# Kernel tuning notes

Hardware: AMD Instinct MI355X
Metric: run time of the kernel (lower is better)

Reference implementation:

```python
import jax, jax.numpy as jnp
import numpy as np

B, D, T, H, CHUNK, MAX_REL = 4, 512, 8192, 8, 64, 2
HD = D // H


def setup_inputs() -> dict:
    key = jax.random.key(0)
    ks = jax.random.split(key, 16)
    s = 0.02
    inp = {
        "q": jax.random.normal(ks[0], (B, D, T), jnp.float32),
        "k": jax.random.normal(ks[1], (B, D, T), jnp.float32),
        "v": jax.random.normal(ks[2], (B, D, T), jnp.float32),
        "masks": jnp.ones((B, 1, T), jnp.float32),
        "Wq": jax.random.normal(ks[3], (D, D), jnp.float32) * s,
        "bq": jnp.zeros((D,), jnp.float32),
        "Wk": jax.random.normal(ks[4], (D, D), jnp.float32) * s,
        "bk": jnp.zeros((D,), jnp.float32),
        "Wv": jax.random.normal(ks[5], (D, D), jnp.float32) * s,
        "bv": jnp.zeros((D,), jnp.float32),
        "Wo": jax.random.normal(ks[6], (D, D), jnp.float32) * s,
        "bo": jnp.zeros((D,), jnp.float32),
        "rel_k": jax.random.normal(ks[7], (2 * MAX_REL + 1, HD), jnp.float32) * s,
        "rel_v": jax.random.normal(ks[8], (2 * MAX_REL + 1, HD), jnp.float32) * s,
    }
    return inp


def reference(q, k, v, masks, Wq, bq, Wk, bk, Wv, bv, Wo, bo, rel_k, rel_v):
    n = CHUNK
    g = T // n  # T is a multiple of chunck_size -> no padding branch
    bg = B * g

    # (B, D, T) -> (B, T, D) -> (B*g, n, D) chunking
    qt = jnp.swapaxes(q, 1, 2).reshape(bg, n, D)
    kt = jnp.swapaxes(k, 1, 2).reshape(bg, n, D)
    vt = jnp.swapaxes(v, 1, 2).reshape(bg, n, D)
    cm = jnp.swapaxes(masks, 1, 2).reshape(bg, n)  # per-chunk mask values

    # gen_key_padding_mask: chunks that are entirely zero are un-masked (set to 1)
    all_zero = jnp.sum(cm, axis=-1) == 0.0
    cm_fixed = jnp.where(all_zero[:, None], 1.0, cm)
    kpm = cm_fixed == 0.0  # (bg, n) True = masked key

    # projections (torch Linear: x @ W.T + b)
    qp = qt @ Wq.T + bq
    kp = kt @ Wk.T + bk
    vp = vt @ Wv.T + bv

    qh = qp.reshape(bg, n, H, HD).transpose(0, 2, 1, 3)  # (bg, H, n, hd)
    kh = kp.reshape(bg, n, H, HD).transpose(0, 2, 1, 3)
    vh = vp.reshape(bg, n, H, HD).transpose(0, 2, 1, 3)

    # content-content scores
    attn1 = jnp.einsum('bhqd,bhkd->bhqk', qh, kh)

    # relative position indices: clip(k - q, -max, max) + max
    ridx = jnp.clip(jnp.arange(n)[None, :] - jnp.arange(n)[:, None], -MAX_REL, MAX_REL) + MAX_REL
    rk = rel_k[ridx]  # (n, n, hd)
    rv = rel_v[ridx]  # (n, n, hd)

    # content-position scores
    attn2 = jnp.einsum('bhqd,qkd->bhqk', qh, rk)

    scale = jnp.sqrt(jnp.asarray(HD, jnp.float32))
    attn = (attn1 + attn2) / scale
    attn = jnp.where(kpm[:, None, None, :], -jnp.inf, attn)
    p = jax.nn.softmax(attn, axis=-1)  # (bg, H, n, n)

    w1 = jnp.einsum('bhqk,bhkd->bhqd', p, vh)
    w2 = jnp.einsum('bhqk,qkd->bhqd', p, rv)
    xo = (w1 + w2).transpose(0, 2, 1, 3).reshape(bg, n, D)
    xo = xo @ Wo.T + bo

    out = xo.reshape(B, T, D)
    out = jnp.swapaxes(out, 1, 2)  # (B, D, T)
    return out * masks
```

## Files before the change

kernel.cpp:

```cpp
#include <hip/hip_runtime.h>


typedef __attribute__((ext_vector_type(8))) short short8;
typedef __attribute__((ext_vector_type(4))) float f32x4;
typedef __attribute__((ext_vector_type(2))) unsigned int uint2v;
typedef __attribute__((ext_vector_type(4))) unsigned short ushort4v;

#define DEV static __device__ __forceinline__

DEV unsigned short f2bf(float f) {
  union { float f; unsigned int u; } x; x.f = f;
  unsigned int r = x.u + 0x7fffu + ((x.u >> 16) & 1u);
  return (unsigned short)(r >> 16);
}
DEV float bf2f(unsigned short h) {
  union { unsigned int u; float f; } x; x.u = ((unsigned int)h) << 16;
  return x.f;
}

DEV void gload16(char* lds, const void* g) {
  __builtin_amdgcn_global_load_lds(
      (const __attribute__((address_space(1))) unsigned int*)g,
      (__attribute__((address_space(3))) unsigned int*)lds, 16, 0, 0);
}

constexpr int Bn = 4, Dm = 512, Tn = 8192, NC = 64;
constexpr int Gn = Tn / NC;
constexpr int BG = Bn * Gn;
constexpr int WSZ = Dm * Dm;
constexpr size_t XTSZ = (size_t)Bn * Tn * Dm;

__global__ __launch_bounds__(256) void wcvt3_tiled(
    const float* __restrict__ wq, const float* __restrict__ wk,
    const float* __restrict__ wv, unsigned short* __restrict__ dst) {
  int i = blockIdx.x * 256 + threadIdx.x;
  int m = i >> 16, fi = i & 65535;
  int o = fi >> 7, d = (fi & 127) << 2;
  const float* src = (m == 0) ? wq : (m == 1) ? wk : wv;
  f32x4 v = *(const f32x4*)(src + o * Dm + d);
  ushort4v u;
  u[0] = f2bf(v[0]); u[1] = f2bf(v[1]); u[2] = f2bf(v[2]); u[3] = f2bf(v[3]);
  int doff = m * WSZ + ((o >> 6) << 15) + ((d >> 5) << 11) + ((o & 63) << 5) + (d & 31);
  *(ushort4v*)(dst + doff) = u;
}

__global__ __launch_bounds__(256) void wcvt_row1(
    const float* __restrict__ wo, unsigned short* __restrict__ dst) {
  int i = (blockIdx.x * 256 + threadIdx.x) * 4;
  f32x4 v = *(const f32x4*)(wo + i);
  ushort4v u;
  u[0] = f2bf(v[0]); u[1] = f2bf(v[1]); u[2] = f2bf(v[2]); u[3] = f2bf(v[3]);
  *(ushort4v*)(dst + i) = u;
}

__global__ __launch_bounds__(256) void wcvt_tiled(
    const float* __restrict__ wq, const float* __restrict__ wk,
    const float* __restrict__ wv, const float* __restrict__ wo,
    unsigned short* __restrict__ dst) {
  int i = blockIdx.x * 256 + threadIdx.x;
  int m = i >> 16, fi = i & 65535;
  int o = fi >> 7, d = (fi & 127) << 2;
  const float* src = (m == 0) ? wq : (m == 1) ? wk : (m == 2) ? wv : wo;
  f32x4 v = *(const f32x4*)(src + o * Dm + d);
  ushort4v u;
  u[0] = f2bf(v[0]); u[1] = f2bf(v[1]); u[2] = f2bf(v[2]); u[3] = f2bf(v[3]);
  int doff = m * WSZ + ((o >> 6) << 15) + ((d >> 5) << 11) + ((o & 63) << 5) + (d & 31);
  *(ushort4v*)(dst + doff) = u;
}

__global__ __launch_bounds__(256) void xpose_kernel(
    const float* __restrict__ q, const float* __restrict__ k,
    const float* __restrict__ v, unsigned short* __restrict__ xt) {
  __shared__ unsigned short tile[64 * 65];
  const int tid = threadIdx.x, bid = blockIdx.x;
  const int tz = bid >> 12, rem = bid & 4095;
  const int cid = rem >> 3, dh = rem & 7;
  const int b = cid >> 7, t0 = (cid & 127) * 64, d0 = dh * 64;
  const float* xin = (tz == 0) ? q : (tz == 1) ? k : v;
  const int lane = tid & 63, drow = tid >> 6;
  const size_t base = (size_t)b * Dm * Tn + t0 + lane;
#pragma unroll
  for (int p = 0; p < 16; ++p) {
    int dr = drow + p * 4;
    float f = xin[base + (size_t)(d0 + dr) * Tn];
    tile[lane * 65 + dr] = f2bf(f);
  }
  __syncthreads();
  unsigned short* xb = xt + (size_t)tz * XTSZ + ((size_t)cid << 15) + (dh << 12);
  const int t = tid >> 2, dlo = (tid & 3) * 8;
#pragma unroll
  for (int h = 0; h < 2; ++h) {
    short8 s;
#pragma unroll
    for (int j = 0; j < 8; ++j) s[j] = (short)tile[t * 65 + h * 32 + dlo + j];
    *(short8*)(xb + h * 2048 + t * 32 + dlo) = s;
  }
}

__global__ __launch_bounds__(512, 4)
void qkvproj4_kernel(const float* __restrict__ qx, const float* __restrict__ kx,
                     const float* __restrict__ vx,
                     const unsigned short* __restrict__ wt3,
                     const float* __restrict__ bq, const float* __restrict__ bk,
                     const float* __restrict__ bv,
                     unsigned short* __restrict__ qkvf)
{
  __shared__ char st[65536];
  const int tid = threadIdx.x;
  const int lane = tid & 63, w = tid >> 6;
  const int l15 = lane & 15, lg = lane >> 4;
  const int bid = blockIdx.x;
  const int mat = bid >> 9;
  const int c = bid & 511;
  const int b = c >> 7, t0 = (c & 127) * 64;
  const float* xin = (mat == 0) ? qx : (mat == 1) ? kx : vx;

  const size_t xbase = (size_t)b * Dm * Tn + t0 + lane;
#pragma unroll
  for (int half = 0; half < 2; ++half) {
    float xr[32];
#pragma unroll
    for (int s = 0; s < 4; ++s)
#pragma unroll
      for (int j = 0; j < 8; ++j)
        xr[s * 8 + j] = xin[xbase + (size_t)((half * 4 + s) * 64 + w * 8 + j) * Tn];
#pragma unroll
    for (int s = 0; s < 4; ++s) {
      int d0 = (half * 4 + s) * 64 + w * 8;
      short8 pk;
#pragma unroll
      for (int j = 0; j < 8; ++j) pk[j] = (short)f2bf(xr[s * 8 + j]);
      int off = (lane * 1024 + d0 * 2) ^ ((lane & 15) << 4);
      *(short8*)(st + off) = pk;
    }
  }
  __syncthreads();

  const int h = w;
  const unsigned short* wb = wt3 + (size_t)mat * WSZ + ((size_t)h << 15);
  const int aoff = l15 * 32 + lg * 8;

  f32x4 acc[4][4];
  const f32x4 fzero = {0.f, 0.f, 0.f, 0.f};
#pragma unroll
  for (int mi = 0; mi < 4; ++mi)
#pragma unroll
    for (int ni = 0; ni < 4; ++ni) acc[mi][ni] = fzero;

  short8 bcur[4], bnxt[4];
#pragma unroll
  for (int ni = 0; ni < 4; ++ni)
    bcur[ni] = *(const short8*)(wb + 0 * 2048 + ni * 512 + aoff);

#pragma unroll
  for (int kk = 0; kk < 16; ++kk) {
    if (kk < 15) {
#pragma unroll
      for (int ni = 0; ni < 4; ++ni)
        bnxt[ni] = *(const short8*)(wb + (kk + 1) * 2048 + ni * 512 + aoff);
    }
    short8 af[4];
#pragma unroll
    for (int mi = 0; mi < 4; ++mi) {
      int t = mi * 16 + l15;
      int off = (t * 1024 + (kk * 32 + lg * 8) * 2) ^ ((t & 15) << 4);
      af[mi] = *(const short8*)(st + off);
    }
#pragma unroll
    for (int ni = 0; ni < 4; ++ni)
#pragma unroll
      for (int mi = 0; mi < 4; ++mi)
        acc[mi][ni] = __builtin_amdgcn_mfma_f32_16x16x32_bf16(af[mi], bcur[ni],
                                                              acc[mi][ni], 0, 0, 0);
#pragma unroll
    for (int ni = 0; ni < 4; ++ni) bcur[ni] = bnxt[ni];
  }
  __syncthreads();

  char* ep = st + w * 8192;
  const float* bias = (mat == 0) ? bq : (mat == 1) ? bk : bv;

  if (mat < 2) {
#pragma unroll
    for (int ni = 0; ni < 4; ++ni) {
      float bi = bias[h * 64 + ni * 16 + l15];
      int hd = ni * 16 + l15;
#pragma unroll
      for (int mi = 0; mi < 4; ++mi)
#pragma unroll
        for (int rr = 0; rr < 4; ++rr) {
          int t = mi * 16 + lg * 4 + rr;
          int off = (t * 128 + hd * 2) ^ ((t & 7) << 4);
          *(unsigned short*)(ep + off) = f2bf(acc[mi][ni][rr] + bi);
        }
    }
  } else {
#pragma unroll
    for (int ni = 0; ni < 4; ++ni) {
      float bi = bias[h * 64 + ni * 16 + l15];
      int hd = ni * 16 + l15;
#pragma unroll
      for (int mi = 0; mi < 4; ++mi) {
        unsigned int lo = (unsigned int)f2bf(acc[mi][ni][0] + bi) |
                          ((unsigned int)f2bf(acc[mi][ni][1] + bi) << 16);
        unsigned int hi = (unsigned int)f2bf(acc[mi][ni][2] + bi) |
                          ((unsigned int)f2bf(acc[mi][ni][3] + bi) << 16);
        uint2v pk; pk[0] = lo; pk[1] = hi;
        int tt = mi * 16 + lg * 4;
        int off = (hd * 128 + tt * 2) ^ ((hd & 7) << 4);
        *(uint2v*)(ep + off) = pk;
      }
    }
  }

  unsigned short* dst = qkvf + (size_t)mat * XTSZ + ((size_t)(c * 8 + h) << 12);
#pragma unroll
  for (int it = 0; it < 8; ++it) {
    int p = it * 64 + lane;
    int row = p >> 3, c16 = p & 7;
    short8 val = *(const short8*)(ep + ((row * 128 + c16 * 16) ^ ((row & 7) << 4)));
    *(short8*)(dst + row * 64 + c16 * 8) = val;
  }
}

__global__ __launch_bounds__(64, 3)
void attn3_kernel(const unsigned short* __restrict__ qkvf,
                  const float* __restrict__ masks,
                  const float* __restrict__ relk, const float* __restrict__ relv,
                  unsigned short* __restrict__ xo)
{
  __shared__ char ldsbuf[16384];
  char* regA = ldsbuf;
  char* regB = ldsbuf + 8192;
  const int lane = threadIdx.x;
  const int l15 = lane & 15, lg = lane >> 4;
  const int bid = blockIdx.x;
  const int c = bid >> 3, h = bid & 7;
  const int b = c >> 7, t0 = (c & 127) * 64;
  const size_t base = (size_t)(c * 8 + h) << 12;
  const unsigned short* qp = qkvf + base;
  const unsigned short* kp = qkvf + XTSZ + base;
  const unsigned short* vp = qkvf + 2 * XTSZ + base;

  float cmv = masks[(size_t)b * Tn + t0 + lane];
  unsigned long long nzb = __ballot(cmv != 0.0f);
  unsigned long long kpm = (nzb == 0ull) ? 0ull : __ballot(cmv == 0.0f);

  const f32x4 fzero = {0.f, 0.f, 0.f, 0.f};

#pragma unroll
  for (int it = 0; it < 8; ++it) {
    int p = it * 64 + lane;
    int row = p >> 3, c16 = p & 7;
    int off = (row * 128 + c16 * 16) ^ ((row & 7) << 4);
    *(short8*)(regA + off) = *(const short8*)(qp + row * 64 + c16 * 8);
    *(short8*)(regB + off) = *(const short8*)(kp + row * 64 + c16 * 8);
  }

  f32x4 sacc[4][4];
#pragma unroll
  for (int mi = 0; mi < 4; ++mi)
#pragma unroll
    for (int ni = 0; ni < 4; ++ni) sacc[mi][ni] = fzero;
#pragma unroll
  for (int kk = 0; kk < 2; ++kk) {
    short8 aq[4], bkf[4];
#pragma unroll
    for (int mi = 0; mi < 4; ++mi) {
      int t = mi * 16 + l15;
      int off = (t * 128 + (kk * 32 + lg * 8) * 2) ^ ((t & 7) << 4);
      aq[mi]  = *(const short8*)(regA + off);
      bkf[mi] = *(const short8*)(regB + off);
    }
#pragma unroll
    for (int ni = 0; ni < 4; ++ni)
#pragma unroll
      for (int mi = 0; mi < 4; ++mi)
        sacc[mi][ni] = __builtin_amdgcn_mfma_f32_16x16x32_bf16(aq[mi], bkf[ni], sacc[mi][ni], 0, 0, 0);
  }

  float qr0 = 0, qr1 = 0, qr2 = 0, qr3 = 0, qr4 = 0;
#pragma unroll
  for (int g = 0; g < 8; ++g) {
    short8 q8 = *(const short8*)(regA + ((lane * 128 + g * 16) ^ ((lane & 7) << 4)));
#pragma unroll
    for (int j = 0; j < 8; ++j) {
      float qf = bf2f((unsigned short)q8[j]);
      qr0 += qf * relk[0 * 64 + g * 8 + j];
      qr1 += qf * relk[1 * 64 + g * 8 + j];
      qr2 += qf * relk[2 * 64 + g * 8 + j];
      qr3 += qf * relk[3 * 64 + g * 8 + j];
      qr4 += qf * relk[4 * 64 + g * 8 + j];
    }
  }

#pragma unroll
  for (int it = 0; it < 8; ++it) {
    int p = it * 64 + lane;
    int row = p >> 3, c16 = p & 7;
    int off = (row * 128 + c16 * 16) ^ ((row & 7) << 4);
    *(short8*)(regA + off) = *(const short8*)(vp + row * 64 + c16 * 8);
  }

  const float scale = 0.125f;
#pragma unroll
  for (int mi = 0; mi < 4; ++mi)
#pragma unroll
    for (int rr = 0; rr < 4; ++rr) {
      int qt = mi * 16 + lg * 4 + rr;
      float q0 = __shfl(qr0, qt), q1 = __shfl(qr1, qt), q2 = __shfl(qr2, qt),
            q3 = __shfl(qr3, qt), q4 = __shfl(qr4, qt);
      float sv[4];
#pragma unroll
      for (int ni = 0; ni < 4; ++ni) {
        int kt = ni * 16 + l15;
        int dd = kt - qt;
        float a2 = (dd <= -2) ? q0 : (dd == -1) ? q1 : (dd == 0) ? q2 : (dd == 1) ? q3 : q4;
        float s = (sacc[mi][ni][rr] + a2) * scale;
        if ((kpm >> kt) & 1ull) s = -1e30f;
        sv[ni] = s;
      }
      float m = fmaxf(fmaxf(sv[0], sv[1]), fmaxf(sv[2], sv[3]));
#pragma unroll
      for (int xm = 1; xm < 16; xm <<= 1) m = fmaxf(m, __shfl_xor(m, xm));
      float ssum = 0.f;
#pragma unroll
      for (int ni = 0; ni < 4; ++ni) { sv[ni] = __expf(sv[ni] - m); ssum += sv[ni]; }
#pragma unroll
      for (int xm = 1; xm < 16; xm <<= 1) ssum += __shfl_xor(ssum, xm);
      float inv = 1.0f / ssum;
#pragma unroll
      for (int ni = 0; ni < 4; ++ni) {
        int kt = ni * 16 + l15;
        int off = (qt * 128 + kt * 2) ^ ((qt & 7) << 4);
        *(unsigned short*)(regB + off) = f2bf(sv[ni] * inv);
      }
    }

  float ps0 = 0, ps1 = 0, ps2 = 0, ps3 = 0, tot = 0;
#pragma unroll
  for (int g = 0; g < 8; ++g) {
    short8 p8 = *(const short8*)(regB + ((lane * 128 + g * 16) ^ ((lane & 7) << 4)));
#pragma unroll
    for (int j = 0; j < 8; ++j) {
      int kt = g * 8 + j;
      float p = bf2f((unsigned short)p8[j]);
      int dd = kt - lane;
      tot += p;
      ps0 += (dd <= -2) ? p : 0.f;
      ps1  = (dd == -1) ? p : ps1;
      ps2  = (dd ==  0) ? p : ps2;
      ps3  = (dd ==  1) ? p : ps3;
    }
  }
  float ps4 = tot - ps0 - ps1 - ps2 - ps3;

  f32x4 oacc[4][4];
#pragma unroll
  for (int mi = 0; mi < 4; ++mi)
#pragma unroll
    for (int ni = 0; ni < 4; ++ni) oacc[mi][ni] = fzero;
#pragma unroll
  for (int kk = 0; kk < 2; ++kk) {
    short8 av[4], bp[4];
#pragma unroll
    for (int mi = 0; mi < 4; ++mi) {
      int row = mi * 16 + l15;
      int off = (row * 128 + (kk * 32 + lg * 8) * 2) ^ ((row & 7) << 4);
      av[mi] = *(const short8*)(regA + off);
      bp[mi] = *(const short8*)(regB + off);
    }
#pragma unroll
    for (int ni = 0; ni < 4; ++ni)
#pragma unroll
      for (int mi = 0; mi < 4; ++mi)
        oacc[mi][ni] = __builtin_amdgcn_mfma_f32_16x16x32_bf16(av[mi], bp[ni], oacc[mi][ni], 0, 0, 0);
  }

  float psh0[4], psh1[4], psh2[4], psh3[4], psh4[4];
#pragma unroll
  for (int ni = 0; ni < 4; ++ni) {
    int qt2 = ni * 16 + l15;
    psh0[ni] = __shfl(ps0, qt2); psh1[ni] = __shfl(ps1, qt2); psh2[ni] = __shfl(ps2, qt2);
    psh3[ni] = __shfl(ps3, qt2); psh4[ni] = __shfl(ps4, qt2);
  }
#pragma unroll
  for (int mi = 0; mi < 4; ++mi) {
    float rv_[4][5];
#pragma unroll
    for (int rr = 0; rr < 4; ++rr) {
      int hd = mi * 16 + lg * 4 + rr;
#pragma unroll
      for (int r = 0; r < 5; ++r) rv_[rr][r] = relv[r * 64 + hd];
    }
#pragma unroll
    for (int ni = 0; ni < 4; ++ni) {
      unsigned short u[4];
#pragma unroll
      for (int rr = 0; rr < 4; ++rr) {
        float w2 = psh0[ni] * rv_[rr][0] + psh1[ni] * rv_[rr][1] + psh2[ni] * rv_[rr][2]
                 + psh3[ni] * rv_[rr][3] + psh4[ni] * rv_[rr][4];
        u[rr] = f2bf(oacc[mi][ni][rr] + w2);
      }
      uint2v pk; pk[0] = u[0] | ((unsigned int)u[1] << 16);
      pk[1] = u[2] | ((unsigned int)u[3] << 16);
      int t = ni * 16 + l15;
      int off = (t * 128 + (mi * 16 + lg * 4) * 2) ^ ((t & 7) << 4);
      *(uint2v*)(regB + off) = pk;
    }
  }

#pragma unroll
  for (int it = 0; it < 8; ++it) {
    int p = it * 64 + lane;
    int row = p >> 3, c16 = p & 7;
    short8 val = *(const short8*)(regB + ((row * 128 + c16 * 16) ^ ((row & 7) << 4)));
    *(short8*)(xo + (size_t)(c * 64 + row) * Dm + h * 64 + c16 * 8) = val;
  }
}

__global__ __launch_bounds__(256, 2)
void outgemm_kernel(const unsigned short* __restrict__ xo,
                    const unsigned short* __restrict__ wo,
                    const float* __restrict__ masks, const float* __restrict__ bo,
                    float* __restrict__ out)
{
  __shared__ char lA[16384], lB[16384];
  const int tid = threadIdx.x;
  const int lane = tid & 63, w = tid >> 6;
  const int wm = w >> 1, wn = w & 1;
  const int l15 = lane & 15, lg = lane >> 4;
  const int bidx = blockIdx.x;
  const int n0 = (bidx & 3) * 128, m0 = (bidx >> 2) * 128;

  f32x4 acc[4][4];
  const f32x4 fzero = {0.f, 0.f, 0.f, 0.f};
#pragma unroll
  for (int mi = 0; mi < 4; ++mi)
#pragma unroll
    for (int ni = 0; ni < 4; ++ni) acc[mi][ni] = fzero;

  for (int k0 = 0; k0 < 512; k0 += 64) {
#pragma unroll
    for (int it = 0; it < 4; ++it) {
      int slot = it * 256 + w * 64 + lane;
      int row = slot >> 3, c16 = slot & 7;
      int gcol = k0 + ((c16 ^ (row & 7)) * 8);
      gload16(lA + it * 4096 + w * 1024, xo + (size_t)(m0 + row) * Dm + gcol);
      gload16(lB + it * 4096 + w * 1024, wo + (size_t)(n0 + row) * Dm + gcol);
    }
    __syncthreads();
#pragma unroll
    for (int kk = 0; kk < 2; ++kk) {
      short8 af[4], bf_[4];
#pragma unroll
      for (int mi = 0; mi < 4; ++mi) {
        int m = wm * 64 + mi * 16 + l15;
        af[mi] = *(const short8*)(lA + ((m * 128 + (kk * 32 + lg * 8) * 2) ^ ((m & 7) << 4)));
      }
#pragma unroll
      for (int ni = 0; ni < 4; ++ni) {
        int n = wn * 64 + ni * 16 + l15;
        bf_[ni] = *(const short8*)(lB + ((n * 128 + (kk * 32 + lg * 8) * 2) ^ ((n & 7) << 4)));
      }
#pragma unroll
      for (int ni = 0; ni < 4; ++ni)
#pragma unroll
        for (int mi = 0; mi < 4; ++mi)
          acc[mi][ni] = __builtin_amdgcn_mfma_f32_16x16x32_bf16(af[mi], bf_[ni], acc[mi][ni], 0, 0, 0);
    }
    __syncthreads();
  }

#pragma unroll
  for (int mi = 0; mi < 4; ++mi) {
    int tg = m0 + wm * 64 + mi * 16 + lg * 4;
    int b = tg >> 13, t = tg & (Tn - 1);
    f32x4 mv = *(const f32x4*)(masks + (size_t)b * Tn + t);
#pragma unroll
    for (int ni = 0; ni < 4; ++ni) {
      int o = n0 + wn * 64 + ni * 16 + l15;
      float bia = bo[o];
      f32x4 r;
#pragma unroll
      for (int rr = 0; rr < 4; ++rr) r[rr] = (acc[mi][ni][rr] + bia) * mv[rr];
      *(f32x4*)(out + ((size_t)b * Dm + o) * Tn + t) = r;
    }
  }
}

__global__ __launch_bounds__(512, 2)
void fused2_kernel(const unsigned short* __restrict__ xt,
                   const float* __restrict__ masks,
                   const unsigned short* __restrict__ wbf,
                   const float* __restrict__ bq, const float* __restrict__ bk,
                   const float* __restrict__ bv, const float* __restrict__ bo,
                   const float* __restrict__ relk, const float* __restrict__ relv,
                   float* __restrict__ out)
{
  extern __shared__ char lds[];
  const int tid  = threadIdx.x;
  const int lane = tid & 63;
  const int w    = tid >> 6;
  const int l15  = lane & 15;
  const int lg   = lane >> 4;
  const int c    = blockIdx.x;
  const int b    = c >> 7;
  const int t0   = (c & (Gn - 1)) * NC;

  char* regA = lds + w * 16384;
  char* regB = regA + 8192;

  float cmv = masks[(size_t)b * Tn + t0 + lane];
  unsigned long long nzb = __ballot(cmv != 0.0f);
  unsigned long long kpm = (nzb == 0ull) ? 0ull : __ballot(cmv == 0.0f);

  const f32x4 fzero = {0.f, 0.f, 0.f, 0.f};
  const int aoff = l15 * 32 + lg * 8;
  const unsigned short* xq = xt + ((size_t)c << 15);
  const unsigned short* xk = xq + XTSZ;
  const unsigned short* xv = xq + 2 * XTSZ;

  auto project = [&](const unsigned short* __restrict__ xb,
                     const unsigned short* __restrict__ wb, f32x4 (&acc)[4][4]) {
#pragma unroll
    for (int mi = 0; mi < 4; ++mi)
#pragma unroll
      for (int ni = 0; ni < 4; ++ni) acc[mi][ni] = fzero;
#pragma unroll
    for (int kk = 0; kk < 16; ++kk) {
      short8 af[4], bf_[4];
#pragma unroll
      for (int mi = 0; mi < 4; ++mi)
        af[mi] = *(const short8*)(xb + kk * 2048 + mi * 512 + aoff);
#pragma unroll
      for (int ni = 0; ni < 4; ++ni)
        bf_[ni] = *(const short8*)(wb + kk * 2048 + ni * 512 + aoff);
#pragma unroll
      for (int ni = 0; ni < 4; ++ni)
#pragma unroll
        for (int mi = 0; mi < 4; ++mi)
          acc[mi][ni] = __builtin_amdgcn_mfma_f32_16x16x32_bf16(af[mi], bf_[ni],
                                                                acc[mi][ni], 0, 0, 0);
    }
  };

  f32x4 acc[4][4];

  project(xq, wbf + 0 * WSZ + w * 32768, acc);
#pragma unroll
  for (int ni = 0; ni < 4; ++ni) {
    float bia = bq[64 * w + ni * 16 + l15];
    int hd = ni * 16 + l15;
#pragma unroll
    for (int mi = 0; mi < 4; ++mi)
#pragma unroll
      for (int rr = 0; rr < 4; ++rr) {
        int t = mi * 16 + lg * 4 + rr;
        int off = (t * 128 + hd * 2) ^ ((t & 7) << 4);
        *(unsigned short*)(regA + off) = f2bf(acc[mi][ni][rr] + bia);
      }
  }

  project(xk, wbf + 1 * WSZ + w * 32768, acc);
#pragma unroll
  for (int ni = 0; ni < 4; ++ni) {
    float bia = bk[64 * w + ni * 16 + l15];
    int hd = ni * 16 + l15;
#pragma unroll
    for (int mi = 0; mi < 4; ++mi)
#pragma unroll
      for (int rr = 0; rr < 4; ++rr) {
        int t = mi * 16 + lg * 4 + rr;
        int off = (t * 128 + hd * 2) ^ ((t & 7) << 4);
        *(unsigned short*)(regB + off) = f2bf(acc[mi][ni][rr] + bia);
      }
  }

  f32x4 sacc[4][4];
#pragma unroll
  for (int mi = 0; mi < 4; ++mi)
#pragma unroll
    for (int ni = 0; ni < 4; ++ni) sacc[mi][ni] = fzero;
#pragma unroll
  for (int kk = 0; kk < 2; ++kk) {
    short8 aq[4], bkf[4];
#pragma unroll
    for (int mi = 0; mi < 4; ++mi) {
      int t = mi * 16 + l15;
      int off = (t * 128 + (kk * 32 + lg * 8) * 2) ^ ((t & 7) << 4);
      aq[mi]  = *(const short8*)(regA + off);
      bkf[mi] = *(const short8*)(regB + off);
    }
#pragma unroll
    for (int ni = 0; ni < 4; ++ni)
#pragma unroll
      for (int mi = 0; mi < 4; ++mi)
        sacc[mi][ni] = __builtin_amdgcn_mfma_f32_16x16x32_bf16(aq[mi], bkf[ni],
                                                               sacc[mi][ni], 0, 0, 0);
  }

  float qr0 = 0, qr1 = 0, qr2 = 0, qr3 = 0, qr4 = 0;
#pragma unroll
  for (int g = 0; g < 8; ++g) {
    short8 q8 = *(const short8*)(regA + ((lane * 128 + g * 16) ^ ((lane & 7) << 4)));
#pragma unroll
    for (int j = 0; j < 8; ++j) {
      float qf = bf2f((unsigned short)q8[j]);
      qr0 += qf * relk[0 * 64 + g * 8 + j];
      qr1 += qf * relk[1 * 64 + g * 8 + j];
      qr2 += qf * relk[2 * 64 + g * 8 + j];
      qr3 += qf * relk[3 * 64 + g * 8 + j];
      qr4 += qf * relk[4 * 64 + g * 8 + j];
    }
  }

  const float scale = 0.125f;
#pragma unroll
  for (int mi = 0; mi < 4; ++mi)
#pragma unroll
    for (int rr = 0; rr < 4; ++rr) {
      int qt = mi * 16 + lg * 4 + rr;
      float q0 = __shfl(qr0, qt), q1 = __shfl(qr1, qt), q2 = __shfl(qr2, qt),
            q3 = __shfl(qr3, qt), q4 = __shfl(qr4, qt);
      float sv[4];
#pragma unroll
      for (int ni = 0; ni < 4; ++ni) {
        int kt = ni * 16 + l15;
        int dd = kt - qt;
        float a2 = (dd <= -2) ? q0 : (dd == -1) ? q1 : (dd == 0) ? q2 : (dd == 1) ? q3 : q4;
        float s = (sacc[mi][ni][rr] + a2) * scale;
        if ((kpm >> kt) & 1ull) s = -1e30f;
        sv[ni] = s;
      }
      float m = fmaxf(fmaxf(sv[0], sv[1]), fmaxf(sv[2], sv[3]));
#pragma unroll
      for (int xm = 1; xm < 16; xm <<= 1) m = fmaxf(m, __shfl_xor(m, xm));
      float ssum = 0.f;
#pragma unroll
      for (int ni = 0; ni < 4; ++ni) { sv[ni] = __expf(sv[ni] - m); ssum += sv[ni]; }
#pragma unroll
      for (int xm = 1; xm < 16; xm <<= 1) ssum += __shfl_xor(ssum, xm);
      float inv = 1.0f / ssum;
#pragma unroll
      for (int ni = 0; ni < 4; ++ni) {
        int kt = ni * 16 + l15;
        int off = (qt * 128 + kt * 2) ^ ((qt & 7) << 4);
        *(unsigned short*)(regB + off) = f2bf(sv[ni] * inv);
      }
    }

  float ps0 = 0, ps1 = 0, ps2 = 0, ps3 = 0, tot = 0;
#pragma unroll
  for (int g = 0; g < 8; ++g) {
    short8 p8 = *(const short8*)(regB + ((lane * 128 + g * 16) ^ ((lane & 7) << 4)));
#pragma unroll
    for (int j = 0; j < 8; ++j) {
      int kt = g * 8 + j;
      float p = bf2f((unsigned short)p8[j]);
      int dd = kt - lane;
      tot += p;
      ps0 += (dd <= -2) ? p : 0.f;
      ps1  = (dd == -1) ? p : ps1;
      ps2  = (dd ==  0) ? p : ps2;
      ps3  = (dd ==  1) ? p : ps3;
    }
  }
  float ps4 = tot - ps0 - ps1 - ps2 - ps3;

  project(xv, wbf + 2 * WSZ + w * 32768, acc);
#pragma unroll
  for (int ni = 0; ni < 4; ++ni) {
    float bia = bv[64 * w + ni * 16 + l15];
    int hd = ni * 16 + l15;
#pragma unroll
    for (int mi = 0; mi < 4; ++mi) {
      unsigned int lo = (unsigned int)f2bf(acc[mi][ni][0] + bia) |
                        ((unsigned int)f2bf(acc[mi][ni][1] + bia) << 16);
      unsigned int hi = (unsigned int)f2bf(acc[mi][ni][2] + bia) |
                        ((unsigned int)f2bf(acc[mi][ni][3] + bia) << 16);
      uint2v pk; pk[0] = lo; pk[1] = hi;
      int off = (hd * 128 + (mi * 16 + lg * 4) * 2) ^ ((hd & 7) << 4);
      *(uint2v*)(regA + off) = pk;
    }
  }

  f32x4 oacc[4][4];
#pragma unroll
  for (int mi = 0; mi < 4; ++mi)
#pragma unroll
    for (int ni = 0; ni < 4; ++ni) oacc[mi][ni] = fzero;
#pragma unroll
  for (int kk = 0; kk < 2; ++kk) {
    short8 av[4], bp[4];
#pragma unroll
    for (int mi = 0; mi < 4; ++mi) {
      int row = mi * 16 + l15;
      int off = (row * 128 + (kk * 32 + lg * 8) * 2) ^ ((row & 7) << 4);
      av[mi] = *(const short8*)(regA + off);
      bp[mi] = *(const short8*)(regB + off);
    }
#pragma unroll
    for (int ni = 0; ni < 4; ++ni)
#pragma unroll
      for (int mi = 0; mi < 4; ++mi)
        oacc[mi][ni] = __builtin_amdgcn_mfma_f32_16x16x32_bf16(av[mi], bp[ni],
                                                               oacc[mi][ni], 0, 0, 0);
  }

  float psh0[4], psh1[4], psh2[4], psh3[4], psh4[4];
#pragma unroll
  for (int ni = 0; ni < 4; ++ni) {
    int qt2 = ni * 16 + l15;
    psh0[ni] = __shfl(ps0, qt2); psh1[ni] = __shfl(ps1, qt2); psh2[ni] = __shfl(ps2, qt2);
    psh3[ni] = __shfl(ps3, qt2); psh4[ni] = __shfl(ps4, qt2);
  }
  uint2v xop[4][4];
#pragma unroll
  for (int mi = 0; mi < 4; ++mi) {
    float rv_[4][5];
#pragma unroll
    for (int rr = 0; rr < 4; ++rr) {
      int hd = mi * 16 + lg * 4 + rr;
#pragma unroll
      for (int r = 0; r < 5; ++r) rv_[rr][r] = relv[r * 64 + hd];
    }
#pragma unroll
    for (int ni = 0; ni < 4; ++ni) {
      unsigned short u[4];
#pragma unroll
      for (int rr = 0; rr < 4; ++rr) {
        float w2 = psh0[ni] * rv_[rr][0] + psh1[ni] * rv_[rr][1] + psh2[ni] * rv_[rr][2]
                 + psh3[ni] * rv_[rr][3] + psh4[ni] * rv_[rr][4];
        u[rr] = f2bf(oacc[mi][ni][rr] + w2);
      }
      uint2v pk; pk[0] = u[0] | ((unsigned int)u[1] << 16);
      pk[1] = u[2] | ((unsigned int)u[3] << 16);
      xop[mi][ni] = pk;
    }
  }

  __syncthreads();
  char* xobuf = lds;
#pragma unroll
  for (int ni = 0; ni < 4; ++ni) {
    int t = ni * 16 + l15;
#pragma unroll
    for (int mi = 0; mi < 4; ++mi) {
      int d = 64 * w + mi * 16 + lg * 4;
      int off = (t * 1024 + d * 2) ^ ((t & 15) << 4);
      *(uint2v*)(xobuf + off) = xop[mi][ni];
    }
  }
  __syncthreads();

  f32x4 cacc[4][4];
#pragma unroll
  for (int mi = 0; mi < 4; ++mi)
#pragma unroll
    for (int ni = 0; ni < 4; ++ni) cacc[mi][ni] = fzero;
  const unsigned short* wob = wbf + 3 * WSZ + w * 32768;
#pragma unroll
  for (int kk = 0; kk < 16; ++kk) {
    short8 ax[4], bw[4];
#pragma unroll
    for (int mi = 0; mi < 4; ++mi) {
      int t = mi * 16 + l15;
      int off = (t * 1024 + (kk * 32 + lg * 8) * 2) ^ ((t & 15) << 4);
      ax[mi] = *(const short8*)(xobuf + off);
    }
#pragma unroll
    for (int ni = 0; ni < 4; ++ni)
      bw[ni] = *(const short8*)(wob + kk * 2048 + ni * 512 + l15 * 32 + lg * 8);
#pragma unroll
    for (int ni = 0; ni < 4; ++ni)
#pragma unroll
      for (int mi = 0; mi < 4; ++mi)
        cacc[mi][ni] = __builtin_amdgcn_mfma_f32_16x16x32_bf16(ax[mi], bw[ni],
                                                               cacc[mi][ni], 0, 0, 0);
  }
#pragma unroll
  for (int mi = 0; mi < 4; ++mi) {
    int tl = mi * 16 + lg * 4;
    f32x4 mv = *(const f32x4*)(masks + (size_t)b * Tn + t0 + tl);
#pragma unroll
    for (int ni = 0; ni < 4; ++ni) {
      int o = 64 * w + ni * 16 + l15;
      float bia = bo[o];
      f32x4 r;
#pragma unroll
      for (int rr = 0; rr < 4; ++rr) r[rr] = (cacc[mi][ni][rr] + bia) * mv[rr];
      *(f32x4*)(out + ((size_t)b * Dm + o) * Tn + t0 + tl) = r;
    }
  }
}

extern "C" void kernel_launch(void* const* d_in, const int* in_sizes, int n_in,
                              void* d_out, int out_size, void* d_ws, size_t ws_size,
                              hipStream_t stream) {
  (void)in_sizes; (void)n_in; (void)out_size;
  const float* q  = (const float*)d_in[0];
  const float* k  = (const float*)d_in[1];
  const float* v  = (const float*)d_in[2];
  const float* ms = (const float*)d_in[3];
  const float* Wq = (const float*)d_in[4];
  const float* bq = (const float*)d_in[5];
  const float* Wk = (const float*)d_in[6];
  const float* bk = (const float*)d_in[7];
  const float* Wv = (const float*)d_in[8];
  const float* bv = (const float*)d_in[9];
  const float* Wo = (const float*)d_in[10];
  const float* bo = (const float*)d_in[11];
  const float* rk = (const float*)d_in[12];
  const float* rv = (const float*)d_in[13];
  float* out = (float*)d_out;

  const size_t needNew = ((size_t)4 * WSZ + 4 * XTSZ) * 2;

  if (ws_size >= needNew) {
    unsigned short* wt3   = (unsigned short*)d_ws;
    unsigned short* worow = wt3 + 3 * WSZ;
    unsigned short* qkvf  = worow + WSZ;
    unsigned short* xo    = qkvf + 3 * XTSZ;
    wcvt3_tiled<<<dim3(768), dim3(256), 0, stream>>>(Wq, Wk, Wv, wt3);
    wcvt_row1<<<dim3(256), dim3(256), 0, stream>>>(Wo, worow);
    qkvproj4_kernel<<<dim3(1536), dim3(512), 0, stream>>>(q, k, v, wt3,
                                                          bq, bk, bv, qkvf);
    attn3_kernel<<<dim3(4096), dim3(64), 0, stream>>>(qkvf, ms, rk, rv, xo);
    outgemm_kernel<<<dim3(1024), dim3(256), 0, stream>>>(xo, worow, ms, bo, out);
  } else {
    unsigned short* wbf = (unsigned short*)d_ws;
    unsigned short* xt = wbf + 4 * WSZ;
    wcvt_tiled<<<dim3(1024), dim3(256), 0, stream>>>(Wq, Wk, Wv, Wo, wbf);
    xpose_kernel<<<dim3(12288), dim3(256), 0, stream>>>(q, k, v, xt);
    hipFuncSetAttribute((const void*)fused2_kernel,
                        hipFuncAttributeMaxDynamicSharedMemorySize, 131072);
    fused2_kernel<<<dim3(BG), dim3(512), 131072, stream>>>(xt, ms, wbf,
                                                           bq, bk, bv, bo, rk, rv, out);
  }
}
```

Measured before the change: 201.9 us.

## Split input transpose into separate kernel and load bf16 tiles via LDS DMA

```diff
diff --git a/kernel.cpp b/kernel.cpp
--- a/kernel.cpp
+++ b/kernel.cpp
@@ -97,42 +97,28 @@
   }
 }
 
-__global__ __launch_bounds__(512, 4)
-void qkvproj4_kernel(const float* __restrict__ qx, const float* __restrict__ kx,
-                     const float* __restrict__ vx,
+__global__ __launch_bounds__(512, 2)
+void qkvproj7_kernel(const unsigned short* __restrict__ xt,
                      const unsigned short* __restrict__ wt3,
                      const float* __restrict__ bq, const float* __restrict__ bk,
                      const float* __restrict__ bv,
                      unsigned short* __restrict__ qkvf)
 {
-  __shared__ char st[65536];
+  __shared__ char St[65536];
   const int tid = threadIdx.x;
   const int lane = tid & 63, w = tid >> 6;
   const int l15 = lane & 15, lg = lane >> 4;
   const int bid = blockIdx.x;
   const int mat = bid >> 9;
   const int c = bid & 511;
-  const int b = c >> 7, t0 = (c & 127) * 64;
-  const float* xin = (mat == 0) ? qx : (mat == 1) ? kx : vx;
-
-  const size_t xbase = (size_t)b * Dm * Tn + t0 + lane;
-#pragma unroll
-  for (int half = 0; half < 2; ++half) {
-    float xr[32];
-#pragma unroll
-    for (int s = 0; s < 4; ++s)
-#pragma unroll
-      for (int j = 0; j < 8; ++j)
-        xr[s * 8 + j] = xin[xbase + (size_t)((half * 4 + s) * 64 + w * 8 + j) * Tn];
-#pragma unroll
-    for (int s = 0; s < 4; ++s) {
-      int d0 = (half * 4 + s) * 64 + w * 8;
-      short8 pk;
-#pragma unroll
-      for (int j = 0; j < 8; ++j) pk[j] = (short)f2bf(xr[s * 8 + j]);
-      int off = (lane * 1024 + d0 * 2) ^ ((lane & 15) << 4);
-      *(short8*)(st + off) = pk;
-    }
+  const unsigned short* xb = xt + (size_t)mat * XTSZ + ((size_t)c << 15);
+
+#pragma unroll
+  for (int i = 0; i < 8; ++i) {
+    int t = w * 8 + i;
+    int d0 = ((lane * 16) ^ ((t & 15) << 4)) >> 1;
+    gload16(St + (t << 10),
+            xb + ((d0 >> 5) << 11) + t * 32 + (d0 & 31));
   }
   __syncthreads();
 
@@ -164,7 +150,7 @@
     for (int mi = 0; mi < 4; ++mi) {
       int t = mi * 16 + l15;
       int off = (t * 1024 + (kk * 32 + lg * 8) * 2) ^ ((t & 15) << 4);
-      af[mi] = *(const short8*)(st + off);
+      af[mi] = *(const short8*)(St + off);
     }
 #pragma unroll
     for (int ni = 0; ni < 4; ++ni)
@@ -177,7 +163,7 @@
   }
   __syncthreads();
 
-  char* ep = st + w * 8192;
+  char* ep = St + w * 8192;
   const float* bias = (mat == 0) ? bq : (mat == 1) ? bk : bv;
 
   if (mat < 2) {
@@ -815,16 +801,18 @@
   const float* rv = (const float*)d_in[13];
   float* out = (float*)d_out;
 
-  const size_t needNew = ((size_t)4 * WSZ + 4 * XTSZ) * 2;
+  const size_t needNew = ((size_t)4 * WSZ + 6 * XTSZ) * 2;
 
   if (ws_size >= needNew) {
     unsigned short* wt3   = (unsigned short*)d_ws;
     unsigned short* worow = wt3 + 3 * WSZ;
-    unsigned short* qkvf  = worow + WSZ;
-    unsigned short* xo    = qkvf + 3 * XTSZ;
+    unsigned short* xt    = worow + WSZ;
+    unsigned short* qkvf  = xt + 3 * XTSZ;
+    unsigned short* xo    = xt;
     wcvt3_tiled<<<dim3(768), dim3(256), 0, stream>>>(Wq, Wk, Wv, wt3);
     wcvt_row1<<<dim3(256), dim3(256), 0, stream>>>(Wo, worow);
-    qkvproj4_kernel<<<dim3(1536), dim3(512), 0, stream>>>(q, k, v, wt3,
+    xpose_kernel<<<dim3(12288), dim3(256), 0, stream>>>(q, k, v, xt);
+    qkvproj7_kernel<<<dim3(1536), dim3(512), 0, stream>>>(xt, wt3,
                                                           bq, bk, bv, qkvf);
     attn3_kernel<<<dim3(4096), dim3(64), 0, stream>>>(qkvf, ms, rk, rv, xo);
     outgemm_kernel<<<dim3(1024), dim3(256), 0, stream>>>(xo, worow, ms, bo, out);
```

Measured after the change: 247.8 us. +22.7%, slower.
